# Performance work log

Measured on AMD Instinct MI355X. Metric: run time of the kernel, lower is better.

Reference implementation:

```python
import jax, jax.numpy as jnp
import numpy as np

N = 100000
E = 1600000
IN_C = 128
HID = 32
HEADS = 4
OUT_C = 16
G = 128
NEG_SLOPE = 0.2


def setup_inputs() -> dict:
    key = jax.random.key(0)
    ks = jax.random.split(key, 16)
    x = jax.random.normal(ks[0], (N, IN_C), dtype=jnp.float32)
    edge_index = jax.random.randint(ks[1], (2, E), 0, N, dtype=jnp.int64)
    batch = jnp.sort(jax.random.randint(ks[2], (N,), 0, G, dtype=jnp.int64))
    node_weights = jax.random.uniform(ks[3], (N, 1), dtype=jnp.float32)
    s = 1.0 / np.sqrt(IN_C)
    W1 = jax.random.uniform(ks[4], (IN_C, HEADS * HID), jnp.float32, -s, s)
    att_src1 = jax.random.uniform(ks[5], (HEADS, HID), jnp.float32, -s, s)
    att_dst1 = jax.random.uniform(ks[6], (HEADS, HID), jnp.float32, -s, s)
    b1 = jnp.zeros((HEADS * HID,), jnp.float32)
    s2 = 1.0 / np.sqrt(HEADS * HID)
    W2 = jax.random.uniform(ks[7], (HEADS * HID, HID), jnp.float32, -s2, s2)
    att_src2 = jax.random.uniform(ks[8], (1, HID), jnp.float32, -s2, s2)
    att_dst2 = jax.random.uniform(ks[9], (1, HID), jnp.float32, -s2, s2)
    b2 = jnp.zeros((HID,), jnp.float32)
    s3 = 1.0 / np.sqrt(HID)
    fcW = jax.random.uniform(ks[10], (HID, OUT_C), jnp.float32, -s3, s3)
    fcb = jax.random.uniform(ks[11], (OUT_C,), jnp.float32, -s3, s3)
    return {"x": x, "edge_index": edge_index, "batch": batch,
            "node_weights": node_weights,
            "W1": W1, "att_src1": att_src1, "att_dst1": att_dst1, "b1": b1,
            "W2": W2, "att_src2": att_src2, "att_dst2": att_dst2, "b2": b2,
            "fcW": fcW, "fcb": fcb}


def gat_conv(x, src, dst, W, att_src, att_dst, bias, heads, ch, concat):
    n = x.shape[0]
    h = (x @ W).reshape(n, heads, ch)                       # [N,H,C]
    a_src = jnp.sum(h * att_src[None], axis=-1)             # [N,H]
    a_dst = jnp.sum(h * att_dst[None], axis=-1)             # [N,H]
    e = jax.nn.leaky_relu(a_src[src] + a_dst[dst], NEG_SLOPE)  # [E,H]
    # segment softmax over incoming edges of each destination node
    e_max = jax.ops.segment_max(e, dst, num_segments=n)
    ex = jnp.exp(e - e_max[dst])
    denom = jax.ops.segment_sum(ex, dst, num_segments=n)
    alpha = ex / denom[dst]                                 # [E,H]
    msg = h[src] * alpha[..., None]                         # [E,H,C]
    out = jax.ops.segment_sum(msg, dst, num_segments=n)     # [N,H,C]
    if concat:
        out = out.reshape(n, heads * ch)
    else:
        out = out.mean(axis=1)
    return out + bias


def reference(x, edge_index, batch, node_weights,
              W1, att_src1, att_dst1, b1,
              W2, att_src2, att_dst2, b2,
              fcW, fcb):
    n = x.shape[0]
    # PyG GATConv adds self-loops by default
    loop = jnp.arange(n, dtype=edge_index.dtype)
    src = jnp.concatenate([edge_index[0], loop])
    dst = jnp.concatenate([edge_index[1], loop])

    h = x * node_weights
    h = jax.nn.elu(gat_conv(h, src, dst, W1, att_src1, att_dst1, b1, HEADS, HID, True))
    h = jax.nn.elu(gat_conv(h, src, dst, W2, att_src2, att_dst2, b2, 1, HID, False))
    # global mean pool over graphs
    sums = jax.ops.segment_sum(h, batch, num_segments=G)
    cnts = jax.ops.segment_sum(jnp.ones((n,), h.dtype), batch, num_segments=G)
    pooled = sums / jnp.maximum(cnts, 1.0)[:, None]
    return pooled @ fcW + fcb
```

## Files before the change

kernel.cpp:

```cpp
#include <hip/hip_runtime.h>
#include <cstdint>

#define NGRAPH 128
#define NEG 0.2f
#define NB_MAX 512
#define BSH 8
#define BSZ 256
#define CAP 8192
#define RC  6144

typedef unsigned int uint;
typedef unsigned short ushort;
typedef unsigned char uchar;
typedef __attribute__((ext_vector_type(8))) short bf16x8;
typedef __attribute__((ext_vector_type(4))) float f32x4;
typedef __attribute__((ext_vector_type(2))) float f32x2;

union U4B { uint4 u; bf16x8 v; };

__device__ __forceinline__ ushort f2bf(float f) {
  uint u = __float_as_uint(f);
  uint r = (u + 0x7FFF + ((u >> 16) & 1)) >> 16;
  return (ushort)r;
}

__device__ __forceinline__ uint cvtpkbf16(float lo, float hi) {
  uint r;
  asm("v_cvt_pk_bf16_f32 %0, %1, %2" : "=v"(r) : "v"(lo), "v"(hi));
  return r;
}

__device__ __forceinline__ void pkfma(f32x2& acc, f32x2 f, f32x2 w) {
  asm("v_pk_fma_f32 %0, %1, %2, %0" : "+v"(acc) : "v"(f), "v"(w));
}

__device__ __forceinline__ float bperm_f(int addr, float v) {
  return __int_as_float(__builtin_amdgcn_ds_bpermute(addr, __float_as_int(v)));
}
__device__ __forceinline__ int bperm_i(int addr, int v) {
  return __builtin_amdgcn_ds_bpermute(addr, v);
}

__device__ __forceinline__ int wave_incl_scan_i(int v) {
  int lane = threadIdx.x & 63;
#pragma unroll
  for (int off = 1; off < 64; off <<= 1) {
    int u = __shfl_up(v, off, 64);
    if (lane >= off) v += u;
  }
  return v;
}

__global__ void k_bin(const int* __restrict__ ei,
                      const float* __restrict__ W1, const float* __restrict__ W2,
                      ushort* __restrict__ Wt1, ushort* __restrict__ Wt2,
                      int E, int Etot, int NB, int nbin,
                      int* __restrict__ bcur, uint* __restrict__ bbuf) {
  if (blockIdx.x >= (uint)nbin) {
    int t2 = (blockIdx.x - nbin) * 256 + threadIdx.x;
    if (t2 < 16384) {
      int n = t2 >> 7, k = t2 & 127;
      Wt1[t2] = f2bf(W1[k * 128 + n]);
    } else {
      int u = t2 - 16384;
      int n = u >> 7, k = u & 127;
      Wt2[u] = f2bf(W2[k * 32 + n]);
    }
    return;
  }
  __shared__ int h[NB_MAX];
  __shared__ int baseo[NB_MAX];
  __shared__ uint crec[4096];
  __shared__ ushort cbkt[4096];
  int t = threadIdx.x;
  for (int b = t; b < NB; b += 256) h[b] = 0;
  __syncthreads();
  int cbase = blockIdx.x * 4096;
  int cend = min(cbase + 4096, Etot);
  int nch = cend - cbase;
  for (int i = t; i < nch; i += 256) {
    int e = cbase + i;
    int s, d;
    if (e < E) { s = ei[e]; d = ei[E + e]; } else { s = e - E; d = s; }
    int b = d >> BSH;
    crec[i] = ((uint)(d & (BSZ - 1)) << 17) | (uint)s;
    cbkt[i] = (ushort)b;
    atomicAdd(&h[b], 1);
  }
  __syncthreads();
  for (int b = t; b < NB; b += 256) {
    int c = h[b];
    baseo[b] = c ? atomicAdd(&bcur[b], c) : 0;
    h[b] = 0;
  }
  __syncthreads();
  for (int i = t; i < nch; i += 256) {
    int b = cbkt[i];
    int r = atomicAdd(&h[b], 1);
    bbuf[(size_t)b * CAP + baseo[b] + r] = crec[i];
  }
}

__global__ void k_bg(const uint* __restrict__ bbuf, const int* __restrict__ bcur,
                     int NB, int N, int* __restrict__ offs, int* __restrict__ ssrc,
                     const float* __restrict__ x, const ushort* __restrict__ Wt,
                     const float* __restrict__ nw, const float* __restrict__ att_s,
                     const float* __restrict__ att_d, uchar* __restrict__ hb1,
                     float* __restrict__ asrc, float* __restrict__ adst) {
  __shared__ int sst[NB_MAX + 1];
  __shared__ int wsum2[4];
  __shared__ int deg[BSZ];
  __shared__ uint rcache[RC];
  if (blockIdx.x < (uint)NB) {
    int t = threadIdx.x, lane = t & 63, wid = t >> 6;
    int v0 = (2 * t < NB) ? bcur[2 * t] : 0;
    int v1 = (2 * t + 1 < NB) ? bcur[2 * t + 1] : 0;
    int s = v0 + v1;
    int sv = wave_incl_scan_i(s);
    if (lane == 63) wsum2[wid] = sv;
    deg[t] = 0;
    __syncthreads();
    if (t == 0) {
      int r = 0;
#pragma unroll
      for (int k = 0; k < 4; k++) { int x2 = wsum2[k]; wsum2[k] = r; r += x2; }
    }
    __syncthreads();
    int excl = wsum2[wid] + sv - s;
    sst[2 * t] = excl;
    sst[2 * t + 1] = excl + v0;
    if (t == 255) sst[512] = excl + v0 + v1;
    __syncthreads();
    int b = blockIdx.x;
    int ebeg = sst[b], eend = sst[b + 1];
    int cnt = eend - ebeg;
    const uint* brow = bbuf + (size_t)b * CAP;
    for (int i = t; i < cnt; i += BSZ) {
      uint rec = brow[i];
      if (i < RC) rcache[i] = rec;
      atomicAdd(&deg[rec >> 17], 1);
    }
    __syncthreads();
    int v = deg[t];
    int sv2 = wave_incl_scan_i(v);
    if (lane == 63) wsum2[wid] = sv2;
    __syncthreads();
    if (t == 0) {
      int r = 0;
#pragma unroll
      for (int k = 0; k < 4; k++) { int x2 = wsum2[k]; wsum2[k] = r; r += x2; }
    }
    __syncthreads();
    int excl2 = wsum2[wid] + sv2 - v;
    int node = (b << BSH) + t;
    if (node < N) offs[node] = ebeg + excl2;
    if (b == 0 && t == 0) offs[N] = sst[512];
    __syncthreads();
    deg[t] = excl2;
    __syncthreads();
    for (int i = t; i < cnt; i += BSZ) {
      uint rec = (i < RC) ? rcache[i] : brow[i];
      int r = atomicAdd(&deg[rec >> 17], 1);
      ssrc[ebeg + r] = (int)(rec & 0x1FFFF);
    }
    return;
  }
  int bid = blockIdx.x - NB;
  int wv = threadIdx.x >> 6, l = threadIdx.x & 63;
  int lg = l >> 4, lr = l & 15;
  int row0 = bid * 64 + wv * 16;
  int node = row0 + lr;
  bool valid = node < N;
  float sc = valid ? nw[node] : 0.f;
  bf16x8 xfr[4];
  const float* xr = x + (size_t)node * 128;
#pragma unroll
  for (int kc = 0; kc < 4; kc++) {
    float v[8];
    if (valid) {
      float4 q0 = *reinterpret_cast<const float4*>(xr + kc * 32 + lg * 8);
      float4 q1 = *reinterpret_cast<const float4*>(xr + kc * 32 + lg * 8 + 4);
      v[0] = q0.x; v[1] = q0.y; v[2] = q0.z; v[3] = q0.w;
      v[4] = q1.x; v[5] = q1.y; v[6] = q1.z; v[7] = q1.w;
    } else {
#pragma unroll
      for (int j = 0; j < 8; j++) v[j] = 0.f;
    }
    U4B a;
    a.u.x = cvtpkbf16(v[0] * sc, v[1] * sc);
    a.u.y = cvtpkbf16(v[2] * sc, v[3] * sc);
    a.u.z = cvtpkbf16(v[4] * sc, v[5] * sc);
    a.u.w = cvtpkbf16(v[6] * sc, v[7] * sc);
    xfr[kc] = a.v;
  }
  float pS[4] = {}, pD[4] = {};
#pragma unroll
  for (int ct = 0; ct < 8; ct++) {
    f32x4 acc = {0.f, 0.f, 0.f, 0.f};
    const ushort* wrow = Wt + (size_t)(ct * 16 + lr) * 128;
#pragma unroll
    for (int kc = 0; kc < 4; kc++) {
      U4B bfr;
      bfr.u = *reinterpret_cast<const uint4*>(wrow + kc * 32 + lg * 8);
      acc = __builtin_amdgcn_mfma_f32_16x16x32_bf16(bfr.v, xfr[kc], acc, 0, 0, 0);
    }
    int c0 = ct * 16 + lg * 4;
    if (valid) {
      uint u8 = (uint)__builtin_amdgcn_cvt_pk_fp8_f32(acc[0], acc[1], 0, false);
      u8 = (uint)__builtin_amdgcn_cvt_pk_fp8_f32(acc[2], acc[3], u8, true);
      *reinterpret_cast<uint*>(hb1 + (size_t)node * 128 + c0) = u8;
    }
    float4 as4 = *reinterpret_cast<const float4*>(att_s + c0);
    float4 ad4 = *reinterpret_cast<const float4*>(att_d + c0);
    int h = ct >> 1;
    pS[h] += acc[0] * as4.x + acc[1] * as4.y + acc[2] * as4.z + acc[3] * as4.w;
    pD[h] += acc[0] * ad4.x + acc[1] * ad4.y + acc[2] * ad4.z + acc[3] * ad4.w;
  }
#pragma unroll
  for (int off = 16; off < 64; off <<= 1) {
#pragma unroll
    for (int h = 0; h < 4; h++) {
      pS[h] += __shfl_xor(pS[h], off, 64);
      pD[h] += __shfl_xor(pD[h], off, 64);
    }
  }
  if (lg == 0 && valid) {
    *reinterpret_cast<float4*>(asrc + node * 4) = make_float4(pS[0], pS[1], pS[2], pS[3]);
    *reinterpret_cast<float4*>(adst + node * 4) = make_float4(pD[0], pD[1], pD[2], pD[3]);
  }
}

__global__ void k_aggr1(const int* __restrict__ offs, const int* __restrict__ ssrc,
                        const uchar* __restrict__ hb, const float* __restrict__ asrc,
                        const float* __restrict__ adst, const float* __restrict__ bias,
                        const ushort* __restrict__ Wt2, const float* __restrict__ as2,
                        const float* __restrict__ ad2, uchar* __restrict__ hb2,
                        float* __restrict__ asrc2, float* __restrict__ adst2, int N) {
  __shared__ ushort rowl[4][136];
  int tid = threadIdx.x;
  int wv = tid >> 6, l = tid & 63;
  int d = blockIdx.x * 4 + wv;
  int dc = min(d, N - 1);
  int slot = l >> 3;
  int cb = l & 7;
  int h = cb >> 1;
  int hq = l & 3;
  int eidx = l >> 2;
  float adq = adst[dc * 4 + hq];
  int beg = offs[dc], end = offs[dc + 1];
  int endm1 = end - 1;
  const uchar* hbc = hb + cb * 16;
  int bp0 = (slot * 4 + h) << 2;
  int bp1 = bp0 + 128;
  f32x2 a2[8] = {};
  float dsp = 0.f;
  auto ACC = [&](uint4 p, float w) {
    f32x2 wp = {w, w};
    f32x2 f;
    f = __builtin_amdgcn_cvt_pk_f32_fp8(p.x, false); pkfma(a2[0], f, wp);
    f = __builtin_amdgcn_cvt_pk_f32_fp8(p.x, true);  pkfma(a2[1], f, wp);
    f = __builtin_amdgcn_cvt_pk_f32_fp8(p.y, false); pkfma(a2[2], f, wp);
    f = __builtin_amdgcn_cvt_pk_f32_fp8(p.y, true);  pkfma(a2[3], f, wp);
    f = __builtin_amdgcn_cvt_pk_f32_fp8(p.z, false); pkfma(a2[4], f, wp);
    f = __builtin_amdgcn_cvt_pk_f32_fp8(p.z, true);  pkfma(a2[5], f, wp);
    f = __builtin_amdgcn_cvt_pk_f32_fp8(p.w, false); pkfma(a2[6], f, wp);
    f = __builtin_amdgcn_cvt_pk_f32_fp8(p.w, true);  pkfma(a2[7], f, wp);
  };
  for (int base = beg; base < end; base += 32) {
    int eA = base + eidx;
    int eB = eA + 16;
    int sA = ssrc[min(eA, endm1)];
    int sB = ssrc[min(eB, endm1)];
    int s0 = bperm_i(bp0, sA);
    int s1 = bperm_i(bp1, sA);
    int s2 = bperm_i(bp0, sB);
    int s3 = bperm_i(bp1, sB);
    int rem = end - base;
    uint4 p0, p1, p2, p3;
    p0 = *reinterpret_cast<const uint4*>(hbc + (size_t)s0 * 128);
    if (rem > 8)  p1 = *reinterpret_cast<const uint4*>(hbc + (size_t)s1 * 128);
    if (rem > 16) p2 = *reinterpret_cast<const uint4*>(hbc + (size_t)s2 * 128);
    if (rem > 24) p3 = *reinterpret_cast<const uint4*>(hbc + (size_t)s3 * 128);
    float aA = asrc[sA * 4 + hq] + adq;
    float aB = asrc[sB * 4 + hq] + adq;
    aA = fmaxf(aA, aA * NEG);
    aB = fmaxf(aB, aB * NEG);
    float wA = (eA < end) ? __expf(aA) : 0.f;
    float wB = (eB < end) ? __expf(aB) : 0.f;
    dsp += wA + wB;
    float w0 = bperm_f(bp0, wA);
    float w1 = bperm_f(bp1, wA);
    float w2 = bperm_f(bp0, wB);
    float w3 = bperm_f(bp1, wB);
    ACC(p0, w0);
    if (rem > 8)  ACC(p1, w1);
    if (rem > 16) ACC(p2, w2);
    if (rem > 24) ACC(p3, w3);
  }
  dsp += __shfl_xor(dsp, 4, 64);
  dsp += __shfl_xor(dsp, 8, 64);
  dsp += __shfl_xor(dsp, 16, 64);
  dsp += __shfl_xor(dsp, 32, 64);
  float ds = bperm_f(h << 2, dsp);
  int b3 = (l >> 3) & 1, b4 = (l >> 4) & 1, b5 = (l >> 5) & 1;
  float t8[8];
#pragma unroll
  for (int r = 0; r < 8; r++) {
    float av = a2[r >> 1][r & 1];
    float bv = a2[(r + 8) >> 1][r & 1];
    float send = b3 ? av : bv;
    float recv = __shfl_xor(send, 8, 64);
    t8[r] = (b3 ? bv : av) + recv;
  }
  float t4[4];
#pragma unroll
  for (int r = 0; r < 4; r++) {
    float send = b4 ? t8[r] : t8[r + 4];
    float recv = __shfl_xor(send, 16, 64);
    t4[r] = (b4 ? t8[r + 4] : t8[r]) + recv;
  }
  float t2[2];
#pragma unroll
  for (int r = 0; r < 2; r++) {
    float send = b5 ? t4[r] : t4[r + 2];
    float recv = __shfl_xor(send, 32, 64);
    t2[r] = (b5 ? t4[r + 2] : t4[r]) + recv;
  }
  float inv = __builtin_amdgcn_rcpf(ds > 0.f ? ds : 1.f);
  int c0 = cb * 16 + b3 * 8 + b4 * 4 + b5 * 2;
  float2 bi = *reinterpret_cast<const float2*>(bias + c0);
  float r0 = fmaf(t2[0], inv, bi.x);
  float r1 = fmaf(t2[1], inv, bi.y);
  r0 = r0 > 0.f ? r0 : __expf(r0) - 1.f;
  r1 = r1 > 0.f ? r1 : __expf(r1) - 1.f;
  *reinterpret_cast<uint*>(&rowl[wv][c0]) = cvtpkbf16(r0, r1);
  __syncthreads();
  if (wv != 0) return;
  int lg = l >> 4, lr = l & 15;
  int rsel = lr & 3;
  bf16x8 bfrag[4];
#pragma unroll
  for (int kc = 0; kc < 4; kc++) {
    U4B bb;
    bb.u = *reinterpret_cast<const uint4*>(&rowl[rsel][kc * 32 + lg * 8]);
    bfrag[kc] = bb.v;
  }
  int dd = blockIdx.x * 4 + lr;
  bool vs = (lr < 4) && (dd < N);
  float pS = 0.f, pD = 0.f;
#pragma unroll
  for (int ct = 0; ct < 2; ct++) {
    f32x4 acc = {0.f, 0.f, 0.f, 0.f};
    const ushort* wrow = Wt2 + (size_t)(ct * 16 + lr) * 128;
#pragma unroll
    for (int kc = 0; kc < 4; kc++) {
      U4B bfr;
      bfr.u = *reinterpret_cast<const uint4*>(wrow + kc * 32 + lg * 8);
      acc = __builtin_amdgcn_mfma_f32_16x16x32_bf16(bfr.v, bfrag[kc], acc, 0, 0, 0);
    }
    int cg = ct * 16 + lg * 4;
    if (vs) {
      uint u8 = (uint)__builtin_amdgcn_cvt_pk_fp8_f32(acc[0], acc[1], 0, false);
      u8 = (uint)__builtin_amdgcn_cvt_pk_fp8_f32(acc[2], acc[3], u8, true);
      *reinterpret_cast<uint*>(hb2 + (size_t)dd * 32 + cg) = u8;
    }
    float4 as4 = *reinterpret_cast<const float4*>(as2 + cg);
    float4 ad4 = *reinterpret_cast<const float4*>(ad2 + cg);
    pS += acc[0] * as4.x + acc[1] * as4.y + acc[2] * as4.z + acc[3] * as4.w;
    pD += acc[0] * ad4.x + acc[1] * ad4.y + acc[2] * ad4.z + acc[3] * ad4.w;
  }
  pS += __shfl_xor(pS, 16, 64);
  pS += __shfl_xor(pS, 32, 64);
  pD += __shfl_xor(pD, 16, 64);
  pD += __shfl_xor(pD, 32, 64);
  if (vs && lg == 0) { asrc2[dd] = pS; adst2[dd] = pD; }
}

__global__ void k_aggr2(const int* __restrict__ offs, const int* __restrict__ ssrc,
                        const uchar* __restrict__ hb, const float* __restrict__ asrc,
                        const float* __restrict__ adst, const float* __restrict__ bias,
                        float* __restrict__ out, int N) {
  int wid = threadIdx.x >> 6, l = threadIdx.x & 63;
  int d = blockIdx.x * 4 + wid;
  if (d >= N) return;
  int slot = l >> 2;
  int k = l & 3;
  float ad = adst[d];
  int beg = offs[d], end = offs[d + 1];
  int endm1 = end - 1;
  const uchar* hbc = hb + k * 8;
  int bq0 = slot << 2;
  int bq1 = (slot + 16) << 2;
  int bq2 = (slot + 32) << 2;
  int bq3 = (slot + 48) << 2;
  f32x2 a2[4] = {};
  float dsp = 0.f;
  auto ACC2 = [&](uint2 p, float w) {
    f32x2 wp = {w, w};
    f32x2 f;
    f = __builtin_amdgcn_cvt_pk_f32_fp8(p.x, false); pkfma(a2[0], f, wp);
    f = __builtin_amdgcn_cvt_pk_f32_fp8(p.x, true);  pkfma(a2[1], f, wp);
    f = __builtin_amdgcn_cvt_pk_f32_fp8(p.y, false); pkfma(a2[2], f, wp);
    f = __builtin_amdgcn_cvt_pk_f32_fp8(p.y, true);  pkfma(a2[3], f, wp);
  };
  for (int base = beg; base < end; base += 64) {
    int e = base + l;
    int sL = ssrc[min(e, endm1)];
    int s0 = bperm_i(bq0, sL);
    int s1 = bperm_i(bq1, sL);
    int s2 = bperm_i(bq2, sL);
    int s3 = bperm_i(bq3, sL);
    int rem = end - base;
    uint2 p0, p1, p2, p3;
    p0 = *reinterpret_cast<const uint2*>(hbc + (size_t)s0 * 32);
    if (rem > 16) p1 = *reinterpret_cast<const uint2*>(hbc + (size_t)s1 * 32);
    if (rem > 32) p2 = *reinterpret_cast<const uint2*>(hbc + (size_t)s2 * 32);
    if (rem > 48) p3 = *reinterpret_cast<const uint2*>(hbc + (size_t)s3 * 32);
    float xv = asrc[sL] + ad;
    xv = fmaxf(xv, xv * NEG);
    float wL = (e < end) ? __expf(xv) : 0.f;
    dsp += wL;
    float w0 = bperm_f(bq0, wL);
    float w1 = bperm_f(bq1, wL);
    float w2 = bperm_f(bq2, wL);
    float w3 = bperm_f(bq3, wL);
    ACC2(p0, w0);
    if (rem > 16) ACC2(p1, w1);
    if (rem > 32) ACC2(p2, w2);
    if (rem > 48) ACC2(p3, w3);
  }
  dsp += __shfl_xor(dsp, 1, 64);
  dsp += __shfl_xor(dsp, 2, 64);
  dsp += __shfl_xor(dsp, 4, 64);
  dsp += __shfl_xor(dsp, 8, 64);
  dsp += __shfl_xor(dsp, 16, 64);
  dsp += __shfl_xor(dsp, 32, 64);
  int b2 = (l >> 2) & 1, b3 = (l >> 3) & 1, b4 = (l >> 4) & 1;
  float t4[4];
#pragma unroll
  for (int r = 0; r < 4; r++) {
    float av = a2[r >> 1][r & 1];
    float bv = a2[(r + 4) >> 1][r & 1];
    float send = b2 ? av : bv;
    float recv = __shfl_xor(send, 4, 64);
    t4[r] = (b2 ? bv : av) + recv;
  }
  float t2[2];
#pragma unroll
  for (int r = 0; r < 2; r++) {
    float send = b3 ? t4[r] : t4[r + 2];
    float recv = __shfl_xor(send, 8, 64);
    t2[r] = (b3 ? t4[r + 2] : t4[r]) + recv;
  }
  float send = b4 ? t2[0] : t2[1];
  float recv = __shfl_xor(send, 16, 64);
  float t1 = (b4 ? t2[1] : t2[0]) + recv;
  t1 += __shfl_xor(t1, 32, 64);
  if (l < 32) {
    int c = k * 8 + b2 * 4 + b3 * 2 + b4;
    float inv = __builtin_amdgcn_rcpf(dsp > 0.f ? dsp : 1.f);
    float r = fmaf(t1, inv, bias[c]);
    r = r > 0.f ? r : __expf(r) - 1.f;
    out[(size_t)d * 32 + c] = r;
  }
}

__global__ void k_pool_fc(const float* __restrict__ h2, const int* __restrict__ batch,
                          const float* __restrict__ fcW, const float* __restrict__ fcb,
                          float* __restrict__ out, int N) {
  int g = blockIdx.x;
  int lo = 0, hi = N;
  while (lo < hi) { int mid = (lo + hi) >> 1; if (batch[mid] < g) lo = mid + 1; else hi = mid; }
  int beg = lo;
  hi = N;
  while (lo < hi) { int mid = (lo + hi) >> 1; if (batch[mid] < g + 1) lo = mid + 1; else hi = mid; }
  int end = lo;
  int t = threadIdx.x, c = t & 31, sub = t >> 5;
  float acc = 0.f;
  for (int n = beg + sub; n < end; n += 8) acc += h2[(size_t)n * 32 + c];
  __shared__ float red[8][32];
  __shared__ float pooled[32];
  red[sub][c] = acc;
  __syncthreads();
  if (sub == 0) {
    float s = 0.f;
#pragma unroll
    for (int i = 0; i < 8; i++) s += red[i][c];
    float cnt = (float)(end - beg);
    pooled[c] = s / fmaxf(cnt, 1.f);
  }
  __syncthreads();
  if (t < 16) {
    float r = fcb[t];
#pragma unroll
    for (int cc = 0; cc < 32; cc++) r += pooled[cc] * fcW[cc * 16 + t];
    out[g * 16 + t] = r;
  }
}

extern "C" void kernel_launch(void* const* d_in, const int* in_sizes, int n_in,
                              void* d_out, int out_size, void* d_ws, size_t ws_size,
                              hipStream_t stream) {
  const float* x     = (const float*)d_in[0];
  const int*   ei    = (const int*)d_in[1];
  const int*   batch = (const int*)d_in[2];
  const float* nw    = (const float*)d_in[3];
  const float* W1    = (const float*)d_in[4];
  const float* as1w  = (const float*)d_in[5];
  const float* ad1w  = (const float*)d_in[6];
  const float* b1    = (const float*)d_in[7];
  const float* W2    = (const float*)d_in[8];
  const float* as2w  = (const float*)d_in[9];
  const float* ad2w  = (const float*)d_in[10];
  const float* b2    = (const float*)d_in[11];
  const float* fcW   = (const float*)d_in[12];
  const float* fcb   = (const float*)d_in[13];
  float* out = (float*)d_out;

  const int N = in_sizes[0] / 128;
  const int E = in_sizes[1] / 2;
  const int Etot = E + N;
  const int NB = (N + BSZ - 1) >> BSH;

  char* w = (char*)d_ws;
  size_t ofs = 0;
  auto alloc = [&](size_t bytes) {
    char* p = w + ofs;
    ofs += (bytes + 255) & ~(size_t)255;
    return p;
  };
  uchar*  hb1    = (uchar*)alloc((size_t)N * 128);
  uchar*  hb2    = (uchar*)alloc((size_t)N * 32);
  float*  h2     = (float*)alloc((size_t)N * 32 * 4);
  float*  asrc1  = (float*)alloc((size_t)N * 4 * 4);
  float*  adst1  = (float*)alloc((size_t)N * 4 * 4);
  float*  asrc2  = (float*)alloc((size_t)N * 4);
  float*  adst2  = (float*)alloc((size_t)N * 4);
  ushort* Wt1    = (ushort*)alloc(16384 * 2);
  ushort* Wt2    = (ushort*)alloc(4096 * 2);
  int*    bcur   = (int*)alloc((size_t)NB * 4);
  int*    offs   = (int*)alloc((size_t)(N + 1) * 4);
  uint*   bbuf   = (uint*)alloc((size_t)NB * CAP * 4);
  int*    ssrc   = (int*)alloc((size_t)Etot * 4);

  hipMemsetAsync(bcur, 0, (size_t)NB * 4, stream);

  const int nbin = (Etot + 4095) / 4096;
  k_bin<<<nbin + 80, 256, 0, stream>>>(ei, W1, W2, Wt1, Wt2, E, Etot, NB, nbin, bcur, bbuf);

  const int ngemm1 = (N + 63) / 64;
  k_bg<<<NB + ngemm1, 256, 0, stream>>>(bbuf, bcur, NB, N, offs, ssrc,
                                        x, Wt1, nw, as1w, ad1w, hb1, asrc1, adst1);

  k_aggr1<<<(N + 3) / 4, 256, 0, stream>>>(offs, ssrc, hb1, asrc1, adst1, b1,
                                           Wt2, as2w, ad2w, hb2, asrc2, adst2, N);

  k_aggr2<<<(N + 3) / 4, 256, 0, stream>>>(offs, ssrc, hb2, asrc2, adst2, b2, h2, N);

  k_pool_fc<<<NGRAPH, 256, 0, stream>>>(h2, batch, fcW, fcb, out, N);
}
```

Measured before the change: 302.5 us.

## Fuse mean-pool into layer-2 aggregation and interleave features with source scores

Layer-2 node records now pack the fp8 features and the source attention score into one 64-byte row, so the gather fetches both from the same line. The aggregation kernel no longer writes the N×32 fp32 output. It reduces per-graph sums in shared memory and adds them to a small global buffer with atomics, leaving a tiny FC kernel. This removes a full write and re-read of the layer-2 output and a separate pooling pass. In exchange it adds atomic contention, non-deterministic summation order, and doubles the gathered row stride.

```diff
diff --git a/kernel.cpp b/kernel.cpp
--- a/kernel.cpp
+++ b/kernel.cpp
@@ -234,8 +234,8 @@
                         const uchar* __restrict__ hb, const float* __restrict__ asrc,
                         const float* __restrict__ adst, const float* __restrict__ bias,
                         const ushort* __restrict__ Wt2, const float* __restrict__ as2,
-                        const float* __restrict__ ad2, uchar* __restrict__ hb2,
-                        float* __restrict__ asrc2, float* __restrict__ adst2, int N) {
+                        const float* __restrict__ ad2, uchar* __restrict__ rec2,
+                        float* __restrict__ adst2, int N) {
   __shared__ ushort rowl[4][136];
   int tid = threadIdx.x;
   int wv = tid >> 6, l = tid & 63;
@@ -362,7 +362,7 @@
     if (vs) {
       uint u8 = (uint)__builtin_amdgcn_cvt_pk_fp8_f32(acc[0], acc[1], 0, false);
       u8 = (uint)__builtin_amdgcn_cvt_pk_fp8_f32(acc[2], acc[3], u8, true);
-      *reinterpret_cast<uint*>(hb2 + (size_t)dd * 32 + cg) = u8;
+      *reinterpret_cast<uint*>(rec2 + (size_t)dd * 64 + cg) = u8;
     }
     float4 as4 = *reinterpret_cast<const float4*>(as2 + cg);
     float4 ad4 = *reinterpret_cast<const float4*>(ad2 + cg);
@@ -373,22 +373,31 @@
   pS += __shfl_xor(pS, 32, 64);
   pD += __shfl_xor(pD, 16, 64);
   pD += __shfl_xor(pD, 32, 64);
-  if (vs && lg == 0) { asrc2[dd] = pS; adst2[dd] = pD; }
+  if (vs && lg == 0) {
+    *reinterpret_cast<float*>(rec2 + (size_t)dd * 64 + 32) = pS;
+    adst2[dd] = pD;
+  }
 }
 
 __global__ void k_aggr2(const int* __restrict__ offs, const int* __restrict__ ssrc,
-                        const uchar* __restrict__ hb, const float* __restrict__ asrc,
-                        const float* __restrict__ adst, const float* __restrict__ bias,
-                        float* __restrict__ out, int N) {
-  int wid = threadIdx.x >> 6, l = threadIdx.x & 63;
+                        const uchar* __restrict__ rec, const float* __restrict__ adst,
+                        const float* __restrict__ bias, const int* __restrict__ batch,
+                        float* __restrict__ gsum, int N) {
+  __shared__ float sblk[4][32];
+  int tid = threadIdx.x;
+  int wid = tid >> 6, l = tid & 63;
+  if (tid < 128) sblk[tid >> 5][tid & 31] = 0.f;
+  __syncthreads();
   int d = blockIdx.x * 4 + wid;
-  if (d >= N) return;
+  bool valid = d < N;
+  int dc = valid ? d : N - 1;
   int slot = l >> 2;
   int k = l & 3;
-  float ad = adst[d];
-  int beg = offs[d], end = offs[d + 1];
+  float ad = adst[dc];
+  int beg = offs[dc];
+  int end = valid ? offs[dc + 1] : beg;
   int endm1 = end - 1;
-  const uchar* hbc = hb + k * 8;
+  const uchar* rk = rec + k * 8;
   int bq0 = slot << 2;
   int bq1 = (slot + 16) << 2;
   int bq2 = (slot + 32) << 2;
@@ -411,12 +420,13 @@
     int s2 = bperm_i(bq2, sL);
     int s3 = bperm_i(bq3, sL);
     int rem = end - base;
+    float av = *reinterpret_cast<const float*>(rec + (size_t)sL * 64 + 32);
     uint2 p0, p1, p2, p3;
-    p0 = *reinterpret_cast<const uint2*>(hbc + (size_t)s0 * 32);
-    if (rem > 16) p1 = *reinterpret_cast<const uint2*>(hbc + (size_t)s1 * 32);
-    if (rem > 32) p2 = *reinterpret_cast<const uint2*>(hbc + (size_t)s2 * 32);
-    if (rem > 48) p3 = *reinterpret_cast<const uint2*>(hbc + (size_t)s3 * 32);
-    float xv = asrc[sL] + ad;
+    p0 = *reinterpret_cast<const uint2*>(rk + (size_t)s0 * 64);
+    if (rem > 16) p1 = *reinterpret_cast<const uint2*>(rk + (size_t)s1 * 64);
+    if (rem > 32) p2 = *reinterpret_cast<const uint2*>(rk + (size_t)s2 * 64);
+    if (rem > 48) p3 = *reinterpret_cast<const uint2*>(rk + (size_t)s3 * 64);
+    float xv = av + ad;
     xv = fmaxf(xv, xv * NEG);
     float wL = (e < end) ? __expf(xv) : 0.f;
     dsp += wL;
@@ -456,45 +466,46 @@
   float recv = __shfl_xor(send, 16, 64);
   float t1 = (b4 ? t2[1] : t2[0]) + recv;
   t1 += __shfl_xor(t1, 32, 64);
-  if (l < 32) {
+  int gfirst = batch[blockIdx.x * 4];
+  if (l < 32 && valid) {
     int c = k * 8 + b2 * 4 + b3 * 2 + b4;
     float inv = __builtin_amdgcn_rcpf(dsp > 0.f ? dsp : 1.f);
     float r = fmaf(t1, inv, bias[c]);
     r = r > 0.f ? r : __expf(r) - 1.f;
-    out[(size_t)d * 32 + c] = r;
-  }
-}
-
-__global__ void k_pool_fc(const float* __restrict__ h2, const int* __restrict__ batch,
-                          const float* __restrict__ fcW, const float* __restrict__ fcb,
-                          float* __restrict__ out, int N) {
+    int g = batch[dc];
+    int sl = g - gfirst;
+    if (sl < 4) atomicAdd(&sblk[sl][c], r);
+    else atomicAdd(&gsum[g * 32 + c], r);
+  }
+  __syncthreads();
+  if (tid < 128) {
+    int sl = tid >> 5, c = tid & 31;
+    float v = sblk[sl][c];
+    int gg = gfirst + sl;
+    if (v != 0.f && gg < NGRAPH) atomicAdd(&gsum[gg * 32 + c], v);
+  }
+}
+
+__global__ void k_fc(const float* __restrict__ gsum, const int* __restrict__ batch,
+                     const float* __restrict__ fcW, const float* __restrict__ fcb,
+                     float* __restrict__ out, int N) {
   int g = blockIdx.x;
+  int l = threadIdx.x;
   int lo = 0, hi = N;
   while (lo < hi) { int mid = (lo + hi) >> 1; if (batch[mid] < g) lo = mid + 1; else hi = mid; }
   int beg = lo;
   hi = N;
   while (lo < hi) { int mid = (lo + hi) >> 1; if (batch[mid] < g + 1) lo = mid + 1; else hi = mid; }
   int end = lo;
-  int t = threadIdx.x, c = t & 31, sub = t >> 5;
-  float acc = 0.f;
-  for (int n = beg + sub; n < end; n += 8) acc += h2[(size_t)n * 32 + c];
-  __shared__ float red[8][32];
+  float inv = 1.f / fmaxf((float)(end - beg), 1.f);
   __shared__ float pooled[32];
-  red[sub][c] = acc;
-  __syncthreads();
-  if (sub == 0) {
-    float s = 0.f;
-#pragma unroll
-    for (int i = 0; i < 8; i++) s += red[i][c];
-    float cnt = (float)(end - beg);
-    pooled[c] = s / fmaxf(cnt, 1.f);
-  }
-  __syncthreads();
-  if (t < 16) {
-    float r = fcb[t];
-#pragma unroll
-    for (int cc = 0; cc < 32; cc++) r += pooled[cc] * fcW[cc * 16 + t];
-    out[g * 16 + t] = r;
+  if (l < 32) pooled[l] = gsum[g * 32 + l] * inv;
+  __syncthreads();
+  if (l < 16) {
+    float r = fcb[l];
+#pragma unroll
+    for (int cc = 0; cc < 32; cc++) r += pooled[cc] * fcW[cc * 16 + l];
+    out[g * 16 + l] = r;
   }
 }
 
@@ -530,20 +541,20 @@
     return p;
   };
   uchar*  hb1    = (uchar*)alloc((size_t)N * 128);
-  uchar*  hb2    = (uchar*)alloc((size_t)N * 32);
-  float*  h2     = (float*)alloc((size_t)N * 32 * 4);
+  uchar*  rec2   = (uchar*)alloc((size_t)N * 64);
   float*  asrc1  = (float*)alloc((size_t)N * 4 * 4);
   float*  adst1  = (float*)alloc((size_t)N * 4 * 4);
-  float*  asrc2  = (float*)alloc((size_t)N * 4);
   float*  adst2  = (float*)alloc((size_t)N * 4);
   ushort* Wt1    = (ushort*)alloc(16384 * 2);
   ushort* Wt2    = (ushort*)alloc(4096 * 2);
   int*    bcur   = (int*)alloc((size_t)NB * 4);
+  float*  gsum   = (float*)alloc((size_t)NGRAPH * 32 * 4);
   int*    offs   = (int*)alloc((size_t)(N + 1) * 4);
   uint*   bbuf   = (uint*)alloc((size_t)NB * CAP * 4);
   int*    ssrc   = (int*)alloc((size_t)Etot * 4);
 
-  hipMemsetAsync(bcur, 0, (size_t)NB * 4, stream);
+  size_t zlen = (size_t)((char*)gsum - (char*)bcur) + (size_t)NGRAPH * 32 * 4;
+  hipMemsetAsync(bcur, 0, zlen, stream);
 
   const int nbin = (Etot + 4095) / 4096;
   k_bin<<<nbin + 80, 256, 0, stream>>>(ei, W1, W2, Wt1, Wt2, E, Etot, NB, nbin, bcur, bbuf);
@@ -553,9 +564,9 @@
                                         x, Wt1, nw, as1w, ad1w, hb1, asrc1, adst1);
 
   k_aggr1<<<(N + 3) / 4, 256, 0, stream>>>(offs, ssrc, hb1, asrc1, adst1, b1,
-                                           Wt2, as2w, ad2w, hb2, asrc2, adst2, N);
-
-  k_aggr2<<<(N + 3) / 4, 256, 0, stream>>>(offs, ssrc, hb2, asrc2, adst2, b2, h2, N);
-
-  k_pool_fc<<<NGRAPH, 256, 0, stream>>>(h2, batch, fcW, fcb, out, N);
-}
+                                           Wt2, as2w, ad2w, rec2, adst2, N);
+
+  k_aggr2<<<(N + 3) / 4, 256, 0, stream>>>(offs, ssrc, rec2, adst2, b2, batch, gsum, N);
+
+  k_fc<<<NGRAPH, 64, 0, stream>>>(gsum, batch, fcW, fcb, out, N);
+}
```

After: 295.4 us. 1.02x faster.
